# Performance work log

Measured on AMD Instinct MI355X. Metric: run time of the kernel, lower is better.

## Reference

```python
import jax, jax.numpy as jnp
import numpy as np

H = W = 256
N_VERTS = 6890
N_FACES = 13776
CHUNK = 164            # 13776 = 84 * 164
N_CHUNKS = N_FACES // CHUNK
BIG = 1e9
EPS = 1e-8


def _project(cam, verts):
    # weak-perspective: s * (xy + t); flip y into image (raster) space
    xy = cam[:, None, 0:1] * (verts[:, :, :2] + cam[:, None, 1:3])
    return jnp.concatenate([xy[..., 0:1], -xy[..., 1:2], verts[:, :, 2:3]], axis=-1)  # [B,N,3]


def _rasterize(proj, faces):
    """Z-buffered rasterization. proj [B,N,3], faces [F,3] ->
    fim [B,P] int32 (face index, -1 = background), wim [B,P,3] barycentric weights."""
    B = proj.shape[0]
    P = H * W
    tri = proj[:, faces]                                   # [B,F,3,3]
    tri_c = tri.reshape(B, N_CHUNKS, CHUNK, 3, 3).transpose(1, 0, 2, 3, 4)  # [nc,B,C,3,3]
    bases = (jnp.arange(N_CHUNKS) * CHUNK).astype(jnp.int32)
    c = (jnp.arange(H, dtype=jnp.float32) + 0.5) / H * 2.0 - 1.0   # pixel centers in [-1,1]
    py, px = jnp.meshgrid(c, c, indexing='ij')
    px = px.reshape(-1)[None, :, None]                     # [1,P,1]
    py = py.reshape(-1)[None, :, None]

    def step(carry, xs):
        zbuf, fid, wim = carry
        t, base = xs                                       # t [B,CHUNK,3,3]
        v = t[:, None]                                     # [B,1,CHUNK,3,3]
        x0, y0, z0 = v[..., 0, 0], v[..., 0, 1], v[..., 0, 2]
        x1, y1, z1 = v[..., 1, 0], v[..., 1, 1], v[..., 1, 2]
        x2, y2, z2 = v[..., 2, 0], v[..., 2, 1], v[..., 2, 2]
        denom = (y1 - y2) * (x0 - x2) + (x2 - x1) * (y0 - y2)
        inv = 1.0 / jnp.where(jnp.abs(denom) < EPS, 1.0, denom)
        w0 = ((y1 - y2) * (px - x2) + (x2 - x1) * (py - y2)) * inv   # [B,P,CHUNK]
        w1 = ((y2 - y0) * (px - x2) + (x0 - x2) * (py - y2)) * inv
        w2 = 1.0 - w0 - w1
        inside = (w0 >= 0) & (w1 >= 0) & (w2 >= 0) & (jnp.abs(denom) >= EPS)
        depth = jnp.where(inside, w0 * z0 + w1 * z1 + w2 * z2, BIG)
        loc = jnp.argmin(depth, axis=-1)                   # [B,P]
        li = loc[..., None]
        dmin = jnp.take_along_axis(depth, li, -1)[..., 0]
        b0 = jnp.take_along_axis(w0, li, -1)[..., 0]
        b1 = jnp.take_along_axis(w1, li, -1)[..., 0]
        b2 = jnp.take_along_axis(w2, li, -1)[..., 0]
        bsel = jnp.stack([b0, b1, b2], axis=-1)            # [B,P,3]
        upd = dmin < zbuf
        zbuf = jnp.where(upd, dmin, zbuf)
        fid = jnp.where(upd, base + loc.astype(jnp.int32), fid)
        wim = jnp.where(upd[..., None], bsel, wim)
        return (zbuf, fid, wim), None

    init = (jnp.full((B, P), BIG, jnp.float32),
            jnp.full((B, P), -1, jnp.int32),
            jnp.zeros((B, P, 3), jnp.float32))
    (zbuf, fid, wim), _ = jax.lax.scan(step, init, (tri_c, bases))
    return fid, wim


def _grid_sample_border(img, grid):
    # torch.nn.functional.grid_sample(bilinear, padding_mode='border', align_corners=False)
    B, C, Hh, Ww = img.shape
    ix = jnp.clip(((grid[..., 0] + 1.0) * Ww - 1.0) * 0.5, 0.0, Ww - 1.0)
    iy = jnp.clip(((grid[..., 1] + 1.0) * Hh - 1.0) * 0.5, 0.0, Hh - 1.0)
    x0 = jnp.floor(ix); y0 = jnp.floor(iy)
    wx = ix - x0; wy = iy - y0
    x0i = x0.astype(jnp.int32); y0i = y0.astype(jnp.int32)
    x1i = jnp.clip(x0i + 1, 0, Ww - 1); y1i = jnp.clip(y0i + 1, 0, Hh - 1)
    b = jnp.arange(B)[:, None, None]
    Ia = img[b, :, y0i, x0i]   # [B,H,W,C]
    Ib = img[b, :, y0i, x1i]
    Ic = img[b, :, y1i, x0i]
    Id = img[b, :, y1i, x1i]
    out = (Ia * ((1 - wx) * (1 - wy))[..., None] + Ib * (wx * (1 - wy))[..., None]
           + Ic * ((1 - wx) * wy)[..., None] + Id * (wx * wy)[..., None])
    return out.transpose(0, 3, 1, 2)


def setup_inputs() -> dict:
    key = jax.random.key(0)
    k1, k2, k3, k4, k5, k6 = jax.random.split(key, 6)
    B = 2
    return {
        'src_img': jax.random.normal(k1, (B, 3, H, W), jnp.float32),
        'src_cam': jax.random.uniform(k2, (B, 3), jnp.float32),
        'src_vertices': jax.random.normal(k3, (B, N_VERTS, 3), jnp.float32),
        'tgt_cam': jax.random.uniform(k4, (B, 3), jnp.float32),
        'tgt_vertices': jax.random.normal(k5, (B, N_VERTS, 3), jnp.float32),
        'faces': jax.random.randint(k6, (N_FACES, 3), 0, N_VERTS, jnp.int32),
    }


def reference(src_img, src_cam, src_vertices, tgt_cam, tgt_vertices, faces):
    B = src_img.shape[0]
    # source faces -> projected 2D verts; flip y back (matches src_f2verts[...,1] *= -1)
    src_proj = _project(src_cam, src_vertices)
    src_f2v = src_proj[:, faces][..., 0:2]                 # [B,F,3,2]
    src_f2v = src_f2v.at[..., 1].multiply(-1.0)
    # rasterize target mesh -> face-index map + barycentric weight map
    tgt_proj = _project(tgt_cam, tgt_vertices)
    fim, wim = _rasterize(tgt_proj, faces)                 # [B,P], [B,P,3]
    fid_clip = jnp.clip(fim, 0, N_FACES - 1)
    gathered = src_f2v[jnp.arange(B)[:, None], fid_clip]   # [B,P,3,2]
    flow = jnp.sum(wim[..., None] * gathered, axis=2)      # [B,P,2]
    flow = jnp.where((fim >= 0)[..., None], flow, -2.0)    # background off-grid
    flow = flow.reshape(B, H, W, 2)
    return _grid_sample_border(src_img, flow)
```

## Files before the change

kernel.cpp:

```cpp
#include <hip/hip_runtime.h>

#pragma clang fp contract(off)

#define HH 256
#define WW 256
#define NVERTS 6890
#define NFACES 13776
#define RASTN (NFACES + 1)
#define PAD1 14336
#define LISTSTRIDE 13824
#define RCHUNK 32
#define MAXCH 432
#define SLABS 4
#define WSUB 896
#define NITER 14
#define SLABSZ (4 * WSUB)
#define NBLK 2048
#define NBLKSEED 128
#define BIGF 1000000000.0f
#define EPSF 1e-8f

__device__ __forceinline__ float pixc(int i) {
    return __fsub_rn(__fmul_rn(__fdiv_rn(__fadd_rn((float)i, 0.5f), 256.0f), 2.0f), 1.0f);
}

__device__ __forceinline__ unsigned int fsort(float f) {
    unsigned int u = __float_as_uint(f);
    return (u & 0x80000000u) ? ~u : (u | 0x80000000u);
}

__device__ __forceinline__ float funsort(unsigned int u) {
    if (u == 0xFFFFFFFFu) return BIGF;
    unsigned int v = (u & 0x80000000u) ? (u & 0x7FFFFFFFu) : ~u;
    return __uint_as_float(v);
}


__global__ __launch_bounds__(256) void precompute_kernel(
    const float* __restrict__ src_cam, const float* __restrict__ src_verts,
    const float* __restrict__ tgt_cam, const float* __restrict__ tgt_verts,
    const int* __restrict__ faces,
    float4* __restrict__ rast64, float* __restrict__ fz,
    uchar4* __restrict__ pass1,
    float4* __restrict__ eplane,
    float4* __restrict__ flowg,
    unsigned long long* __restrict__ zbuf,
    int* __restrict__ counts, int* __restrict__ done, int* __restrict__ qcount,
    int B)
{
    int idx = blockIdx.x * blockDim.x + threadIdx.x;
    if (idx < B * HH * WW) zbuf[idx] = ~0ull;
    if (counts && idx < B * 256) { counts[idx] = 0; done[idx] = 0; }
    if (qcount && idx == 0) qcount[0] = 0;
    if (idx >= B * PAD1) return;
    int b = idx / PAD1;
    int f = idx - b * PAD1;
    if (f >= NFACES) {
        if (pass1) pass1[(size_t)b * PAD1 + f] = make_uchar4(255, 255, 0, 0);
        if (f == NFACES) {
            float4* rr = rast64 + ((size_t)b * RASTN + f) * 4;
            rr[0] = make_float4(0.0f, 0.0f, 0.0f, 0.0f);
            rr[1] = make_float4(0.0f, 0.0f, 1.0f, __int_as_float(-1));
            rr[2] = make_float4(BIGF, BIGF, BIGF, 0.0f);
            rr[3] = make_float4(0.0f, 0.0f, 0.0f, 0.0f);
            if (fz) fz[(size_t)b * RASTN + f] = BIGF;
        }
        return;
    }
    float4* rr = rast64 + ((size_t)b * RASTN + f) * 4;
    int i0 = faces[3*f+0], i1 = faces[3*f+1], i2 = faces[3*f+2];

    float tc0 = tgt_cam[3*b+0], tc1 = tgt_cam[3*b+1], tc2 = tgt_cam[3*b+2];
    const float* tv = tgt_verts + (size_t)b * NVERTS * 3;
    float x0 = __fmul_rn(tc0, __fadd_rn(tv[3*i0+0], tc1));
    float y0 = -__fmul_rn(tc0, __fadd_rn(tv[3*i0+1], tc2));
    float z0 = tv[3*i0+2];
    float x1 = __fmul_rn(tc0, __fadd_rn(tv[3*i1+0], tc1));
    float y1 = -__fmul_rn(tc0, __fadd_rn(tv[3*i1+1], tc2));
    float z1 = tv[3*i1+2];
    float x2 = __fmul_rn(tc0, __fadd_rn(tv[3*i2+0], tc1));
    float y2 = -__fmul_rn(tc0, __fadd_rn(tv[3*i2+1], tc2));
    float z2 = tv[3*i2+2];

    float A  = __fsub_rn(y1, y2);
    float D  = __fsub_rn(x0, x2);
    float Bc = __fsub_rn(x2, x1);
    float E_ = __fsub_rn(y0, y2);
    float denom = __fadd_rn(__fmul_rn(A, D), __fmul_rn(Bc, E_));
    bool valid = (fabsf(denom) >= EPSF);
    float inv = __fdiv_rn(1.0f, valid ? denom : 1.0f);
    float Cc = __fsub_rn(y2, y0);

    float fzmin = fminf(fminf(z0, z1), z2)
                - 4e-6f * (fabsf(z0) + fabsf(z1) + fabsf(z2)) - 1e-30f;

    if (valid) {
        rr[0] = make_float4(x2, y2, A, Bc);
        rr[1] = make_float4(Cc, D, inv, __int_as_float(f));
        rr[2] = make_float4(z0, z1, z2, 0.0f);
    } else {
        rr[0] = make_float4(0.0f, 0.0f, 0.0f, 0.0f);
        rr[1] = make_float4(0.0f, 0.0f, 1.0f, __int_as_float(f));
        rr[2] = make_float4(BIGF, BIGF, BIGF, 0.0f);
    }
    rr[3] = make_float4(0.0f, 0.0f, 0.0f, 0.0f);
    if (fz) fz[(size_t)b * RASTN + f] = valid ? fzmin : BIGF;

    uchar4 range;
    float4 e1, e2, e3;
    if (valid) {
        float xmn = fminf(fminf(x0, x1), x2), xmx = fmaxf(fmaxf(x0, x1), x2);
        float ymn = fminf(fminf(y0, y1), y2), ymx = fmaxf(fmaxf(y0, y1), y2);
        float S = fmaxf(fmaxf(fabsf(xmn), fabsf(xmx)),
                        fmaxf(fabsf(ymn), fabsf(ymx))) + 1.01f;
        float slop = 2e-6f * S;
        float l0 = sqrtf(D*D + E_*E_);
        float dx1v = x1 - x2, dy1v = y1 - y2;
        float l1 = sqrtf(dx1v*dx1v + dy1v*dy1v);
        float dx2v = x1 - x0, dy2v = y1 - y0;
        float l2 = sqrtf(dx2v*dx2v + dy2v*dy2v);
        float mp = fmaxf(fmaxf(l0*l1, l1*l2), l0*l2);
        float Ex = slop * mp / fabsf(denom);
        float m = Ex + slop + 1e-4f;
        float bxmn = xmn - m, bymn = ymn - m, bxmx = xmx + m, bymx = ymx + m;

        int txlo = (int)floorf((__fmul_rn(__fadd_rn(bxmn, 1.0f), 128.0f) - 15.5f) * 0.0625f);
        txlo = max(0, min(16, txlo));
        while (txlo > 0  && pixc(16*(txlo-1)+15) >= bxmn) txlo--;
        while (txlo < 16 && pixc(16*txlo+15)     <  bxmn) txlo++;
        int txhi = (int)floorf((__fmul_rn(__fadd_rn(bxmx, 1.0f), 128.0f) - 0.5f) * 0.0625f);
        txhi = max(-1, min(15, txhi));
        while (txhi < 15 && pixc(16*(txhi+1)) <= bxmx) txhi++;
        while (txhi >= 0 && pixc(16*txhi)     >  bxmx) txhi--;
        int tylo = (int)floorf((__fmul_rn(__fadd_rn(bymn, 1.0f), 128.0f) - 15.5f) * 0.0625f);
        tylo = max(0, min(16, tylo));
        while (tylo > 0  && pixc(16*(tylo-1)+15) >= bymn) tylo--;
        while (tylo < 16 && pixc(16*tylo+15)     <  bymn) tylo++;
        int tyhi = (int)floorf((__fmul_rn(__fadd_rn(bymx, 1.0f), 128.0f) - 0.5f) * 0.0625f);
        tyhi = max(-1, min(15, tyhi));
        while (tyhi < 15 && pixc(16*(tyhi+1)) <= bymx) tyhi++;
        while (tyhi >= 0 && pixc(16*tyhi)     >  bymx) tyhi--;
        if (txlo > txhi || tylo > tyhi || txlo > 15 || tylo > 15 ||
            txhi < 0 || tyhi < 0) {
            range = make_uchar4(255, 255, 0, 0);
        } else {
            range = make_uchar4((unsigned char)txlo, (unsigned char)tylo,
                                (unsigned char)txhi, (unsigned char)tyhi);
        }

        float s = (denom >= 0.0f) ? 1.0f : -1.0f;
        float gx0 = s * A,  gy0 = s * Bc;
        float gx1 = s * Cc, gy1 = s * D;
        float gx2 = s * (y0 - y1), gy2 = s * (x1 - x0);
        float b0 = -(gx0 * x2 + gy0 * y2);
        float b1 = -(gx1 * x2 + gy1 * y2);
        float b2 = fabsf(denom) - b0 - b1;
        float mm15 = 1.5f * m;
        float k0 = b0 + mm15 * l1 + 1e-6f;
        float k1 = b1 + mm15 * l0 + 1e-6f;
        float k2 = b2 + mm15 * l2 + 1e-6f;
        e1 = make_float4(gx0, gy0, k0, gx1);
        e2 = make_float4(gy1, k1, gx2, gy2);
        e3 = make_float4(k2, 0.0f, 0.0f, 0.0f);
    } else {
        range = make_uchar4(255, 255, 0, 0);
        e1 = make_float4(0.0f, 0.0f, -1.0f, 0.0f);
        e2 = make_float4(0.0f, -1.0f, 0.0f, 0.0f);
        e3 = make_float4(-1.0f, 0.0f, 0.0f, 0.0f);
    }
    if (pass1) pass1[(size_t)b * PAD1 + f] = range;
    if (eplane) {
        float4* ep = eplane + ((size_t)b * NFACES + f) * 4;
        ep[0] = e1; ep[1] = e2; ep[2] = e3;
        ep[3] = make_float4(0.0f, 0.0f, 0.0f, 0.0f);
    }

    float sc0 = src_cam[3*b+0], sc1 = src_cam[3*b+1], sc2 = src_cam[3*b+2];
    const float* sv = src_verts + (size_t)b * NVERTS * 3;
    float g0x = __fmul_rn(sc0, __fadd_rn(sv[3*i0+0], sc1));
    float g0y = __fmul_rn(sc0, __fadd_rn(sv[3*i0+1], sc2));
    float g1x = __fmul_rn(sc0, __fadd_rn(sv[3*i1+0], sc1));
    float g1y = __fmul_rn(sc0, __fadd_rn(sv[3*i1+1], sc2));
    float g2x = __fmul_rn(sc0, __fadd_rn(sv[3*i2+0], sc1));
    float g2y = __fmul_rn(sc0, __fadd_rn(sv[3*i2+1], sc2));
    size_t fo = ((size_t)b * NFACES + f) * 2;
    flowg[fo+0] = make_float4(g0x, g0y, g1x, g1y);
    flowg[fo+1] = make_float4(g2x, g2y, 0.0f, 0.0f);
}

__global__ __launch_bounds__(256) void bin_kernel(
    const uchar4* __restrict__ pass1, const float4* __restrict__ eplane,
    int* __restrict__ lists,
    int* __restrict__ counts, int* __restrict__ done,
    unsigned int* __restrict__ queue, int* __restrict__ qcount, int B)
{
    __shared__ int seg[4][WSUB];
    int tile = blockIdx.x;
    int slab = blockIdx.y;
    int b = blockIdx.z;
    int tileG = b * 256 + tile;
    int tX = tile & 15, tY = tile >> 4;
    float txmin = pixc(tX * 16), txmax = pixc(tX * 16 + 15);
    float tymin = pixc(tY * 16), tymax = pixc(tY * 16 + 15);

    int wv = threadIdx.x >> 6, lane = threadIdx.x & 63;
    const uchar4* p1 = pass1 + (size_t)b * PAD1;
    const float4* ep = eplane + (size_t)b * NFACES * 4;
    int* mylist = lists + (size_t)tileG * LISTSTRIDE;
    int wlo = slab * SLABSZ + wv * WSUB;
    int cnt = 0;

    int f0 = wlo + lane;
    uchar4 c = p1[f0];

    #pragma unroll
    for (int it = 0; it < NITER; ++it) {
        uchar4 n;
        if (it + 1 < NITER) n = p1[f0 + (it + 1) * 64];
        int f = f0 + it * 64;
        bool pass = (tX >= (int)c.x) & (tX <= (int)c.z) &
                    (tY >= (int)c.y) & (tY <= (int)c.w);
        unsigned long long m = __ballot(pass);
        if (pass) {
            int pre = __popcll(m & ((1ull << lane) - 1ull));
            seg[wv][cnt + pre] = f;
        }
        cnt += __popcll(m);
        c = n;
    }

    int outc = 0;
    for (int base = 0; base < cnt; base += 64) {
        int i = base + lane;
        int f = (i < cnt) ? seg[wv][i] : 0;
        const float4* er = ep + (size_t)f * 4;
        float4 e1 = er[0], e2 = er[1], e3 = er[2];
        float v0 = e1.x * (e1.x >= 0.0f ? txmax : txmin)
                 + e1.y * (e1.y >= 0.0f ? tymax : tymin) + e1.z;
        float v1 = e1.w * (e1.w >= 0.0f ? txmax : txmin)
                 + e2.x * (e2.x >= 0.0f ? tymax : tymin) + e2.y;
        float v2 = e2.z * (e2.z >= 0.0f ? txmax : txmin)
                 + e2.w * (e2.w >= 0.0f ? tymax : tymin) + e3.x;
        bool pass = (i < cnt) & (v0 >= 0.0f) & (v1 >= 0.0f) & (v2 >= 0.0f);
        unsigned long long m = __ballot(pass);
        if (pass) {
            int pre = __popcll(m & ((1ull << lane) - 1ull));
            seg[wv][outc + pre] = f;
        }
        outc += __popcll(m);
    }
    cnt = outc;

    int gbase = 0;
    if (lane == 0 && cnt) gbase = atomicAdd(&counts[tileG], cnt);
    gbase = __shfl(gbase, 0);
    for (int i = lane; i < cnt; i += 64) mylist[gbase + i] = seg[wv][i];

    __syncthreads();
    if (threadIdx.x < 64) {
        int isLast = 0, cc = 0;
        if (threadIdx.x == 0) {
            isLast = (atomicAdd(&done[tileG], 1) == SLABS - 1);
            if (isLast) cc = atomicAdd(&counts[tileG], 0);
        }
        isLast = __shfl(isLast, 0);
        if (isLast) {
            cc = __shfl(cc, 0);
            int padded = (cc + RCHUNK - 1) & ~(RCHUNK - 1);
            for (int i = cc + threadIdx.x; i < padded; i += 64)
                mylist[i] = NFACES;
            int nch = padded / RCHUNK;
            if (nch > 1) {
                int qb = 0;
                if (threadIdx.x == 0) qb = atomicAdd(qcount, nch - 1);
                qb = __shfl(qb, 0);
                for (int kk = 1 + threadIdx.x; kk < nch; kk += 64)
                    queue[qb + kk - 1] =
                        ((unsigned int)tileG << 10) | (unsigned int)kk;
            }
            if (threadIdx.x == 0)
                done[tileG] = padded;
        }
    }
}

__global__ __launch_bounds__(256) void raster_kernel(
    const float* __restrict__ rast64, const int* __restrict__ lists,
    const float* __restrict__ fz,
    const unsigned int* __restrict__ queue, const int* __restrict__ donep,
    const int* __restrict__ qcount,
    unsigned long long* __restrict__ zbuf, int B, int seedMode)
{
    int wv = threadIdx.x >> 6, lane = threadIdx.x & 63;
    int waveId = blockIdx.x * 4 + wv;
    int nwaves = gridDim.x * 4;
    int NT = B * 256;
    int qn;
    if (!lists)        qn = B * 256 * MAXCH;
    else if (seedMode) qn = NT;
    else               qn = qcount[0];
    qn = __builtin_amdgcn_readfirstlane(qn);

    for (int e = waveId; e < qn; e += nwaves) {
        int tileG, k;
        if (!lists) {
            tileG = e / MAXCH; k = e - tileG * MAXCH;
        } else if (seedMode) {
            tileG = e; k = 0;
            if (donep[tileG] == 0) continue;
        } else {
            unsigned int ent = queue[e];
            tileG = (int)(ent >> 10); k = (int)(ent & 1023u);
        }
        tileG = __builtin_amdgcn_readfirstlane(tileG);
        k = __builtin_amdgcn_readfirstlane(k);
        const int* lp = lists ? (lists + (size_t)tileG * LISTSTRIDE + k * RCHUNK)
                              : nullptr;
        int b = tileG >> 8, tile = tileG & 255;
        const float* rb = rast64 + (size_t)b * RASTN * 16;

        int tX = tile & 15, tY = tile >> 4;
        int col = lane & 15, row0 = lane >> 4;
        int pxi = tX * 16 + col;
        float px = pixc(pxi);
        int ry0 = tY * 16 + row0;
        float py0 = pixc(ry0);
        float py1 = pixc(ry0 + 4);
        float py2 = pixc(ry0 + 8);
        float py3 = pixc(ry0 + 12);

        unsigned int mask = 0xFFFFFFFFu;
        if (lists && !seedMode) {
            size_t zbase = ((size_t)b << 16) | (size_t)pxi;
            unsigned long long pk0 = __hip_atomic_load(
                &zbuf[zbase | ((size_t)ry0 << 8)],
                __ATOMIC_RELAXED, __HIP_MEMORY_SCOPE_AGENT);
            unsigned long long pk1 = __hip_atomic_load(
                &zbuf[zbase | ((size_t)(ry0 + 4) << 8)],
                __ATOMIC_RELAXED, __HIP_MEMORY_SCOPE_AGENT);
            unsigned long long pk2 = __hip_atomic_load(
                &zbuf[zbase | ((size_t)(ry0 + 8) << 8)],
                __ATOMIC_RELAXED, __HIP_MEMORY_SCOPE_AGENT);
            unsigned long long pk3 = __hip_atomic_load(
                &zbuf[zbase | ((size_t)(ry0 + 12) << 8)],
                __ATOMIC_RELAXED, __HIP_MEMORY_SCOPE_AGENT);
            float lb = fmaxf(fmaxf(funsort((unsigned int)(pk0 >> 32)),
                                   funsort((unsigned int)(pk1 >> 32))),
                             fmaxf(funsort((unsigned int)(pk2 >> 32)),
                                   funsort((unsigned int)(pk3 >> 32))));
            #pragma unroll
            for (int off = 1; off < 64; off <<= 1)
                lb = fmaxf(lb, __shfl_xor(lb, off, 64));
            int fidx = lp[lane & 31];
            float fzv = fz[(size_t)b * RASTN + fidx];
            unsigned long long bm = __ballot((lane < 32) & (fzv <= lb));
            mask = (unsigned int)bm;
            if (mask == 0u) continue;
        }

        float z0c = BIGF, z1c = BIGF, z2c = BIGF, z3c = BIGF;
        int f0c = -1, f1c = -1, f2c = -1, f3c = -1;

        for (int j = 0; j < RCHUNK; j += 4) {
            unsigned int g = (mask >> j) & 0xFu;
            if (!g) continue;
            int4 fis;
            if (lp) {
                fis = *(const int4*)(lp + j);
            } else {
                int base = k * RCHUNK + j;
                fis.x = min(base + 0, NFACES); fis.y = min(base + 1, NFACES);
                fis.z = min(base + 2, NFACES); fis.w = min(base + 3, NFACES);
            }
            #pragma unroll
            for (int q = 0; q < 4; ++q) {
                if (!(g & (1u << q))) continue;
                int fi = (q == 0) ? fis.x : (q == 1) ? fis.y : (q == 2) ? fis.z : fis.w;
                fi = __builtin_amdgcn_readfirstlane(fi);
                const float* r = rb + (size_t)fi * 16;
                float X2 = r[0], Y2 = r[1], A = r[2], Bc = r[3];
                float Cc = r[4], Dd = r[5], inv = r[6];
                int   fid = __float_as_int(r[7]);
                float Z0 = r[8], Z1 = r[9], Z2 = r[10];

                float dx  = __fsub_rn(px, X2);
                float Adx = __fmul_rn(A, dx);
                float Cdx = __fmul_rn(Cc, dx);
                auto evalp = [&](float py, float& zc, int& fc) {
                    float dy = __fsub_rn(py, Y2);
                    float w0 = __fmul_rn(__fadd_rn(Adx, __fmul_rn(Bc, dy)), inv);
                    float w1 = __fmul_rn(__fadd_rn(Cdx, __fmul_rn(Dd, dy)), inv);
                    float w2 = __fsub_rn(__fsub_rn(1.0f, w0), w1);
                    float d  = __fadd_rn(__fadd_rn(__fmul_rn(w0, Z0), __fmul_rn(w1, Z1)),
                                         __fmul_rn(w2, Z2));
                    float mm = fminf(fminf(w0, w1), w2);
                    bool ins = (mm >= 0.0f) & (d < zc);
                    if (ins) { zc = d; fc = fid; }
                };
                evalp(py0, z0c, f0c);
                evalp(py1, z1c, f1c);
                evalp(py2, z2c, f2c);
                evalp(py3, z3c, f3c);
            }
        }

        auto commit = [&](int rowk, float zc, int fc) {
            if (fc >= 0) {
                unsigned long long pk =
                    ((unsigned long long)fsort(zc) << 32) | (unsigned int)fc;
                int pyi = ry0 + rowk * 4;
                atomicMin(&zbuf[((size_t)b << 16) | (pyi << 8) | pxi], pk);
            }
        };
        commit(0, z0c, f0c);
        commit(1, z1c, f1c);
        commit(2, z2c, f2c);
        commit(3, z3c, f3c);
    }
}

__global__ __launch_bounds__(256) void resolve_kernel(
    const float* __restrict__ rast64, const float4* __restrict__ flowg,
    const unsigned long long* __restrict__ zbuf,
    const float* __restrict__ src_img, float* __restrict__ out, int B)
{
    int idx = blockIdx.x * 256 + threadIdx.x;
    if (idx >= B * HH * WW) return;
    int b = idx >> 16;
    int pix = idx & 65535;
    int pxi = pix & 255, pyi = pix >> 8;
    float px = pixc(pxi), py = pixc(pyi);

    unsigned int fid = (unsigned int)zbuf[idx];
    float fx, fy;
    if (fid != 0xFFFFFFFFu) {
        const float* r = rast64 + ((size_t)b * RASTN + fid) * 16;
        float dx = __fsub_rn(px, r[0]);
        float dy = __fsub_rn(py, r[1]);
        float w0 = __fmul_rn(__fadd_rn(__fmul_rn(r[2], dx), __fmul_rn(r[3], dy)), r[6]);
        float w1 = __fmul_rn(__fadd_rn(__fmul_rn(r[4], dx), __fmul_rn(r[5], dy)), r[6]);
        float w2 = __fsub_rn(__fsub_rn(1.0f, w0), w1);
        const float4* fg = flowg + ((size_t)b * NFACES + fid) * 2;
        float4 g0 = fg[0];
        float4 g1 = fg[1];
        fx = __fadd_rn(__fadd_rn(__fmul_rn(w0, g0.x), __fmul_rn(w1, g0.z)),
                       __fmul_rn(w2, g1.x));
        fy = __fadd_rn(__fadd_rn(__fmul_rn(w0, g0.y), __fmul_rn(w1, g0.w)),
                       __fmul_rn(w2, g1.y));
    } else {
        fx = -2.0f; fy = -2.0f;
    }

    float ix = __fmul_rn(__fsub_rn(__fmul_rn(__fadd_rn(fx, 1.0f), 256.0f), 1.0f), 0.5f);
    float iy = __fmul_rn(__fsub_rn(__fmul_rn(__fadd_rn(fy, 1.0f), 256.0f), 1.0f), 0.5f);
    ix = fminf(fmaxf(ix, 0.0f), 255.0f);
    iy = fminf(fmaxf(iy, 0.0f), 255.0f);
    float x0f = floorf(ix), y0f = floorf(iy);
    float wx = __fsub_rn(ix, x0f), wy = __fsub_rn(iy, y0f);
    int x0i = (int)x0f, y0i = (int)y0f;
    int x1i = min(x0i + 1, 255), y1i = min(y0i + 1, 255);
    float omwx = __fsub_rn(1.0f, wx), omwy = __fsub_rn(1.0f, wy);
    float wa = __fmul_rn(omwx, omwy);
    float wb = __fmul_rn(wx, omwy);
    float wc = __fmul_rn(omwx, wy);
    float wd = __fmul_rn(wx, wy);
    const float* img = src_img + (size_t)b * 3 * HH * WW;
    int o00 = y0i * WW + x0i, o01 = y0i * WW + x1i;
    int o10 = y1i * WW + x0i, o11 = y1i * WW + x1i;
    float* ob = out + (size_t)b * 3 * HH * WW + (size_t)pyi * WW + pxi;
    for (int c = 0; c < 3; ++c) {
        const float* ic = img + (size_t)c * HH * WW;
        float Ia = ic[o00], Ib = ic[o01], Ic = ic[o10], Id = ic[o11];
        float val = __fadd_rn(__fadd_rn(__fadd_rn(__fmul_rn(Ia, wa), __fmul_rn(Ib, wb)),
                                        __fmul_rn(Ic, wc)),
                              __fmul_rn(Id, wd));
        ob[(size_t)c * HH * WW] = val;
    }
}

extern "C" void kernel_launch(void* const* d_in, const int* in_sizes, int n_in,
                              void* d_out, int out_size, void* d_ws, size_t ws_size,
                              hipStream_t stream)
{
    const float* src_img   = (const float*)d_in[0];
    const float* src_cam   = (const float*)d_in[1];
    const float* src_verts = (const float*)d_in[2];
    const float* tgt_cam   = (const float*)d_in[3];
    const float* tgt_verts = (const float*)d_in[4];
    const int*   faces     = (const int*)d_in[5];
    int B = in_sizes[1] / 3;

    size_t off = 0;
    auto alloc = [&](size_t bytes) {
        size_t o = off;
        off = (off + bytes + 255) & ~(size_t)255;
        return o;
    };
    size_t rastOff = alloc((size_t)B * RASTN * 64);
    size_t fzOff   = alloc((size_t)B * RASTN * sizeof(float));
    size_t p1Off   = alloc((size_t)B * PAD1 * 4);
    size_t edgOff  = alloc((size_t)B * NFACES * 64);
    size_t flowOff = alloc((size_t)B * NFACES * 2 * sizeof(float4));
    size_t zbufOff = alloc((size_t)B * HH * WW * sizeof(unsigned long long));
    size_t cntOff  = alloc((size_t)B * 256 * sizeof(int));
    size_t donOff  = alloc((size_t)B * 256 * sizeof(int));
    size_t qcOff   = alloc(sizeof(int));
    size_t quOff   = alloc((size_t)B * 256 * MAXCH * sizeof(unsigned int));
    size_t listOff = alloc((size_t)B * 256 * LISTSTRIDE * sizeof(int));
    bool binned = (off <= ws_size);

    char* ws = (char*)d_ws;
    float4* rast64 = (float4*)(ws + rastOff);
    float*  fz     = (float*)(ws + fzOff);
    uchar4* pass1  = binned ? (uchar4*)(ws + p1Off)  : nullptr;
    float4* eplane = binned ? (float4*)(ws + edgOff) : nullptr;
    float4* flowg  = (float4*)(ws + flowOff);
    unsigned long long* zbuf = (unsigned long long*)(ws + zbufOff);
    int* counts = binned ? (int*)(ws + cntOff) : nullptr;
    int* done   = binned ? (int*)(ws + donOff) : nullptr;
    int* qcount = binned ? (int*)(ws + qcOff)  : nullptr;
    unsigned int* queue = binned ? (unsigned int*)(ws + quOff) : nullptr;
    int* lists  = binned ? (int*)(ws + listOff) : nullptr;

    int nInit = B * HH * WW;
    int nPre  = B * PAD1;
    int nMax  = nInit > nPre ? nInit : nPre;
    precompute_kernel<<<(nMax + 255) / 256, 256, 0, stream>>>(
        src_cam, src_verts, tgt_cam, tgt_verts, faces,
        rast64, fz, pass1, eplane, flowg, zbuf, counts, done, qcount, B);
    if (binned) {
        bin_kernel<<<dim3(256, SLABS, B), 256, 0, stream>>>(
            pass1, eplane, lists, counts, done, queue, qcount, B);
        raster_kernel<<<NBLKSEED, 256, 0, stream>>>(
            (const float*)rast64, lists, fz, queue, done, qcount, zbuf, B, 1);
        raster_kernel<<<NBLK, 256, 0, stream>>>(
            (const float*)rast64, lists, fz, queue, done, qcount, zbuf, B, 0);
    } else {
        raster_kernel<<<NBLK, 256, 0, stream>>>(
            (const float*)rast64, nullptr, fz, nullptr, nullptr, nullptr,
            zbuf, B, 0);
    }
    resolve_kernel<<<(B * HH * WW + 255) / 256, 256, 0, stream>>>(
        (const float*)rast64, flowg, zbuf, src_img, (float*)d_out, B);
}
```

Measured before the change: 154.3 us.

## Replace chunk work queue and seed pass with chunk-major grid over tiles

Measured after the change: 239.4 us. 55.1% more time.

```diff
diff --git a/kernel.cpp b/kernel.cpp
--- a/kernel.cpp
+++ b/kernel.cpp
@@ -16,7 +16,7 @@
 #define NITER 14
 #define SLABSZ (4 * WSUB)
 #define NBLK 2048
-#define NBLKSEED 128
+#define NWAVES (NBLK * 4)
 #define BIGF 1000000000.0f
 #define EPSF 1e-8f
 
@@ -192,7 +192,7 @@
     const uchar4* __restrict__ pass1, const float4* __restrict__ eplane,
     int* __restrict__ lists,
     int* __restrict__ counts, int* __restrict__ done,
-    unsigned int* __restrict__ queue, int* __restrict__ qcount, int B)
+    int* __restrict__ qcount, int B)
 {
     __shared__ int seg[4][WSUB];
     int tile = blockIdx.x;
@@ -269,17 +269,11 @@
             int padded = (cc + RCHUNK - 1) & ~(RCHUNK - 1);
             for (int i = cc + threadIdx.x; i < padded; i += 64)
                 mylist[i] = NFACES;
-            int nch = padded / RCHUNK;
-            if (nch > 1) {
-                int qb = 0;
-                if (threadIdx.x == 0) qb = atomicAdd(qcount, nch - 1);
-                qb = __shfl(qb, 0);
-                for (int kk = 1 + threadIdx.x; kk < nch; kk += 64)
-                    queue[qb + kk - 1] =
-                        ((unsigned int)tileG << 10) | (unsigned int)kk;
+            if (threadIdx.x == 0) {
+                int nch = padded / RCHUNK;
+                if (nch) atomicMax(qcount, nch);
+                done[tileG] = padded;
             }
-            if (threadIdx.x == 0)
-                done[tileG] = padded;
         }
     }
 }
@@ -287,35 +281,31 @@
 __global__ __launch_bounds__(256) void raster_kernel(
     const float* __restrict__ rast64, const int* __restrict__ lists,
     const float* __restrict__ fz,
-    const unsigned int* __restrict__ queue, const int* __restrict__ donep,
-    const int* __restrict__ qcount,
-    unsigned long long* __restrict__ zbuf, int B, int seedMode)
+    const int* __restrict__ donep, const int* __restrict__ qcount,
+    unsigned long long* __restrict__ zbuf, int B)
 {
     int wv = threadIdx.x >> 6, lane = threadIdx.x & 63;
     int waveId = blockIdx.x * 4 + wv;
-    int nwaves = gridDim.x * 4;
     int NT = B * 256;
     int qn;
-    if (!lists)        qn = B * 256 * MAXCH;
-    else if (seedMode) qn = NT;
-    else               qn = qcount[0];
+    if (!lists) qn = B * 256 * MAXCH;
+    else        qn = qcount[0] * NT;
     qn = __builtin_amdgcn_readfirstlane(qn);
 
-    for (int e = waveId; e < qn; e += nwaves) {
+    for (int e = waveId; e < qn; e += NWAVES) {
         int tileG, k;
         if (!lists) {
             tileG = e / MAXCH; k = e - tileG * MAXCH;
-        } else if (seedMode) {
-            tileG = e; k = 0;
-            if (donep[tileG] == 0) continue;
         } else {
-            unsigned int ent = queue[e];
-            tileG = (int)(ent >> 10); k = (int)(ent & 1023u);
+            k = e / NT; tileG = e - k * NT;
         }
         tileG = __builtin_amdgcn_readfirstlane(tileG);
         k = __builtin_amdgcn_readfirstlane(k);
-        const int* lp = lists ? (lists + (size_t)tileG * LISTSTRIDE + k * RCHUNK)
-                              : nullptr;
+        const int* lp = nullptr;
+        if (lists) {
+            if (k * RCHUNK >= donep[tileG]) continue;
+            lp = lists + (size_t)tileG * LISTSTRIDE + k * RCHUNK;
+        }
         int b = tileG >> 8, tile = tileG & 255;
         const float* rb = rast64 + (size_t)b * RASTN * 16;
 
@@ -330,7 +320,7 @@
         float py3 = pixc(ry0 + 12);
 
         unsigned int mask = 0xFFFFFFFFu;
-        if (lists && !seedMode) {
+        if (lp) {
             size_t zbase = ((size_t)b << 16) | (size_t)pxi;
             unsigned long long pk0 = __hip_atomic_load(
                 &zbuf[zbase | ((size_t)ry0 << 8)],
@@ -505,7 +495,6 @@
     size_t cntOff  = alloc((size_t)B * 256 * sizeof(int));
     size_t donOff  = alloc((size_t)B * 256 * sizeof(int));
     size_t qcOff   = alloc(sizeof(int));
-    size_t quOff   = alloc((size_t)B * 256 * MAXCH * sizeof(unsigned int));
     size_t listOff = alloc((size_t)B * 256 * LISTSTRIDE * sizeof(int));
     bool binned = (off <= ws_size);
 
@@ -519,7 +508,6 @@
     int* counts = binned ? (int*)(ws + cntOff) : nullptr;
     int* done   = binned ? (int*)(ws + donOff) : nullptr;
     int* qcount = binned ? (int*)(ws + qcOff)  : nullptr;
-    unsigned int* queue = binned ? (unsigned int*)(ws + quOff) : nullptr;
     int* lists  = binned ? (int*)(ws + listOff) : nullptr;
 
     int nInit = B * HH * WW;
@@ -530,15 +518,12 @@
         rast64, fz, pass1, eplane, flowg, zbuf, counts, done, qcount, B);
     if (binned) {
         bin_kernel<<<dim3(256, SLABS, B), 256, 0, stream>>>(
-            pass1, eplane, lists, counts, done, queue, qcount, B);
-        raster_kernel<<<NBLKSEED, 256, 0, stream>>>(
-            (const float*)rast64, lists, fz, queue, done, qcount, zbuf, B, 1);
+            pass1, eplane, lists, counts, done, qcount, B);
         raster_kernel<<<NBLK, 256, 0, stream>>>(
-            (const float*)rast64, lists, fz, queue, done, qcount, zbuf, B, 0);
+            (const float*)rast64, lists, fz, done, qcount, zbuf, B);
     } else {
         raster_kernel<<<NBLK, 256, 0, stream>>>(
-            (const float*)rast64, nullptr, fz, nullptr, nullptr, nullptr,
-            zbuf, B, 0);
+            (const float*)rast64, nullptr, fz, nullptr, nullptr, zbuf, B);
     }
     resolve_kernel<<<(B * HH * WW + 255) / 256, 256, 0, stream>>>(
         (const float*)rast64, flowg, zbuf, src_img, (float*)d_out, B);
```
